# Kernel optimization log

Hardware: AMD Instinct MI355X
Metric: run time of the kernel (lower is better)

## Reference

```python
import jax, jax.numpy as jnp
import numpy as np

B, S, D, DM, H = 2, 2048, 1024, 1024, 16
DH = D // H
EPS = 1e-5


def layernorm(x, g, b):
    m = jnp.mean(x, axis=-1, keepdims=True)
    v = jnp.mean(jnp.square(x - m), axis=-1, keepdims=True)
    return (x - m) * jax.lax.rsqrt(v + EPS) * g + b


def setup_inputs() -> dict:
    key = jax.random.key(0)
    ks = jax.random.split(key, 16)
    std = 0.02
    p = {
        'x': jax.random.normal(ks[0], (B, S, D), jnp.float32),
        'h': jnp.zeros((B, DM), jnp.float32),
        'c': jnp.zeros((B, DM), jnp.float32),
        'Wq': jax.random.normal(ks[1], (D, D), jnp.float32) * std,
        'Wk': jax.random.normal(ks[2], (D, D), jnp.float32) * std,
        'Wv': jax.random.normal(ks[3], (D, D), jnp.float32) * std,
        'Wo': jax.random.normal(ks[4], (D, D), jnp.float32) * std,
        'Wmk': jax.random.normal(ks[5], (DM, D), jnp.float32) * std,
        'Wmv': jax.random.normal(ks[6], (DM, D), jnp.float32) * std,
        'Wih': jax.random.normal(ks[7], (D, 4 * DM), jnp.float32) * std,
        'Whh': jax.random.normal(ks[8], (DM, 4 * DM), jnp.float32) * std,
        'b_ih': jnp.zeros((4 * DM,), jnp.float32),
        'b_hh': jnp.zeros((4 * DM,), jnp.float32),
        'W1': jax.random.normal(ks[9], (D, 4 * D), jnp.float32) * std,
        'bf1': jnp.zeros((4 * D,), jnp.float32),
        'W2': jax.random.normal(ks[10], (4 * D, D), jnp.float32) * std,
        'bf2': jnp.zeros((D,), jnp.float32),
        'g1': jnp.ones((D,), jnp.float32), 'be1': jnp.zeros((D,), jnp.float32),
        'g2': jnp.ones((D,), jnp.float32), 'be2': jnp.zeros((D,), jnp.float32),
        'g3': jnp.ones((D,), jnp.float32), 'be3': jnp.zeros((D,), jnp.float32),
        'Wmp': jax.random.normal(ks[11], (DM, D), jnp.float32) * std,
    }
    return p


def reference(x, h, c, Wq, Wk, Wv, Wo, Wmk, Wmv, Wih, Whh, b_ih, b_hh,
              W1, bf1, W2, bf2, g1, be1, g2, be2, g3, be3, Wmp):
    xn = layernorm(x, g1, be1)
    # projections, split heads: [B,S,D] -> [B,H,S,DH]
    def heads(t):
        return t.reshape(B, -1, H, DH).transpose(0, 2, 1, 3)
    Q = heads(xn @ Wq)
    Ks = heads(xn @ Wk)
    Vs = heads(xn @ Wv)
    Km = (h @ Wmk).reshape(B, 1, H, DH).transpose(0, 2, 1, 3)  # [B,H,1,DH]
    Vm = (h @ Wmv).reshape(B, 1, H, DH).transpose(0, 2, 1, 3)
    K = jnp.concatenate([Km, Ks], axis=2)  # [B,H,S+1,DH]
    V = jnp.concatenate([Vm, Vs], axis=2)
    scores = jnp.einsum('bhqd,bhkd->bhqk', Q, K) / jnp.sqrt(jnp.float32(DH))
    attn = jax.nn.softmax(scores, axis=-1)
    ao = jnp.einsum('bhqk,bhkd->bhqd', attn, V)
    ao = ao.transpose(0, 2, 1, 3).reshape(B, S, D)
    attended = x + ao @ Wo
    # LSTM step on mean-pooled tokens (torch LSTMCell gate order: i,f,g,o)
    pooled = jnp.mean(attended, axis=1)  # [B,D]
    gates = pooled @ Wih + b_ih + h @ Whh + b_hh
    i, f, g, o = jnp.split(gates, 4, axis=-1)
    new_c = jax.nn.sigmoid(f) * c + jax.nn.sigmoid(i) * jnp.tanh(g)
    new_h = jax.nn.sigmoid(o) * jnp.tanh(new_c)
    mixed = attended + (new_h @ Wmp)[:, None, :]
    hn = layernorm(mixed, g2, be2)
    ffn = jax.nn.gelu(hn @ W1 + bf1, approximate=False) @ W2 + bf2
    out = layernorm(mixed + ffn, g3, be3)
    return (out, new_h, new_c)
```

## Files before the change

### kernel.cpp

```cpp
#include <hip/hip_runtime.h>
#include <hip/hip_bf16.h>
#include <math.h>

#define BB 2
#define SS 2048
#define DD 1024
#define HH 16
#define RR (BB*SS)
#define KSTRIDE 2064
#define MB (1024ull*1024ull)

typedef unsigned short u16;
typedef unsigned int u32;
typedef __attribute__((ext_vector_type(8))) short short8v;
typedef __attribute__((ext_vector_type(4))) float f32x4;
typedef __attribute__((ext_vector_type(16))) float f32x16;
typedef __attribute__((ext_vector_type(4))) u16 u16x4;

__device__ __forceinline__ u16 f2bf(float f){
    union { __hip_bfloat16 h; u16 u; } c; c.h = __float2bfloat16(f); return c.u;
}
__device__ __forceinline__ u32 cvtpk(float a, float b){
    u32 r;
    asm("v_cvt_pk_bf16_f32 %0, %1, %2" : "=v"(r) : "v"(a), "v"(b));
    return r;
}
__device__ __forceinline__ float exp2_raw(float x){
    float r;
    asm("v_exp_f32 %0, %1" : "=v"(r) : "v"(x));
    return r;
}
__device__ __forceinline__ float bf2f(u16 u){
    union { u32 i; float f; } c; c.i = (u32)u << 16; return c.f;
}
__device__ __forceinline__ float erf_fast(float x){
    float ax = fabsf(x);
    float t = __builtin_amdgcn_rcpf(1.0f + 0.3275911f*ax);
    float y = t*(0.254829592f + t*(-0.284496736f + t*(1.421413741f + t*(-1.453152027f + t*1.061405429f))));
    float r = 1.0f - y*__expf(-ax*ax);
    return copysignf(r, x);
}

#define GLL16(gp, lp) __builtin_amdgcn_global_load_lds( \
    (const __attribute__((address_space(1))) void*)(gp), \
    (__attribute__((address_space(3))) void*)(lp), 16, 0, 0)

#define VMCNT8 asm volatile("s_waitcnt vmcnt(8)" ::: "memory")
#define VMCNT4 asm volatile("s_waitcnt vmcnt(4)" ::: "memory")
#define VMCNT0 asm volatile("s_waitcnt vmcnt(0)" ::: "memory")
#define SBAR   __builtin_amdgcn_s_barrier()
#define SCHEDB __builtin_amdgcn_sched_barrier(0)

__global__ __launch_bounds__(256) void ln_kernel(const float* __restrict__ in,
    const float* __restrict__ mproj, const float* __restrict__ g, const float* __restrict__ be,
    float* __restrict__ mixed_out, float* __restrict__ outf, u16* __restrict__ outb)
{
    int row = blockIdx.x; int b = row / SS; int tid = threadIdx.x;
    float4 v = ((const float4*)(in + (size_t)row*DD))[tid];
    if (mproj){
        float4 mp = ((const float4*)(mproj + (size_t)b*DD))[tid];
        v.x+=mp.x; v.y+=mp.y; v.z+=mp.z; v.w+=mp.w;
        ((float4*)(mixed_out + (size_t)row*DD))[tid] = v;
    }
    float s = v.x+v.y+v.z+v.w, s2 = v.x*v.x+v.y*v.y+v.z*v.z+v.w*v.w;
    #pragma unroll
    for (int off=32; off>0; off>>=1){ s += __shfl_down(s,off); s2 += __shfl_down(s2,off); }
    __shared__ float red[2][4];
    if ((tid&63)==0){ red[0][tid>>6]=s; red[1][tid>>6]=s2; }
    __syncthreads();
    float st = red[0][0]+red[0][1]+red[0][2]+red[0][3];
    float s2t= red[1][0]+red[1][1]+red[1][2]+red[1][3];
    float mean = st*(1.f/DD); float var = s2t*(1.f/DD)-mean*mean;
    float rs = rsqrtf(var + 1e-5f);
    float4 gg=((const float4*)g)[tid], bb2=((const float4*)be)[tid];
    float o0=(v.x-mean)*rs*gg.x+bb2.x, o1=(v.y-mean)*rs*gg.y+bb2.y;
    float o2=(v.z-mean)*rs*gg.z+bb2.z, o3=(v.w-mean)*rs*gg.w+bb2.w;
    if (outf){ float4 o={o0,o1,o2,o3}; ((float4*)(outf+(size_t)row*DD))[tid]=o; }
    if (outb){ u16x4 o={f2bf(o0),f2bf(o1),f2bf(o2),f2bf(o3)}; ((u16x4*)(outb+(size_t)row*DD))[tid]=o; }
}

__global__ __launch_bounds__(256) void ln3f_kernel(const u16* __restrict__ pb0,
    const u16* __restrict__ pb1, const u16* __restrict__ pb2, const u16* __restrict__ pb3,
    const float* __restrict__ bias, const float* __restrict__ resid,
    const float* __restrict__ g, const float* __restrict__ be, float* __restrict__ out)
{
    int row = blockIdx.x; int tid = threadIdx.x;
    size_t off = (size_t)row*DD;
    u16x4 q0 = ((const u16x4*)(pb0+off))[tid];
    u16x4 q1 = ((const u16x4*)(pb1+off))[tid];
    u16x4 q2 = ((const u16x4*)(pb2+off))[tid];
    u16x4 q3 = ((const u16x4*)(pb3+off))[tid];
    float4 bi = ((const float4*)bias)[tid];
    float4 rs4= ((const float4*)(resid+off))[tid];
    float4 v;
    v.x = bf2f(q0[0])+bf2f(q1[0])+bf2f(q2[0])+bf2f(q3[0]) + bi.x + rs4.x;
    v.y = bf2f(q0[1])+bf2f(q1[1])+bf2f(q2[1])+bf2f(q3[1]) + bi.y + rs4.y;
    v.z = bf2f(q0[2])+bf2f(q1[2])+bf2f(q2[2])+bf2f(q3[2]) + bi.z + rs4.z;
    v.w = bf2f(q0[3])+bf2f(q1[3])+bf2f(q2[3])+bf2f(q3[3]) + bi.w + rs4.w;
    float s = v.x+v.y+v.z+v.w, s2 = v.x*v.x+v.y*v.y+v.z*v.z+v.w*v.w;
    #pragma unroll
    for (int off2=32; off2>0; off2>>=1){ s += __shfl_down(s,off2); s2 += __shfl_down(s2,off2); }
    __shared__ float red[2][4];
    if ((tid&63)==0){ red[0][tid>>6]=s; red[1][tid>>6]=s2; }
    __syncthreads();
    float st = red[0][0]+red[0][1]+red[0][2]+red[0][3];
    float s2t= red[1][0]+red[1][1]+red[1][2]+red[1][3];
    float mean = st*(1.f/DD); float var = s2t*(1.f/DD)-mean*mean;
    float rs = rsqrtf(var + 1e-5f);
    float4 gg=((const float4*)g)[tid], bb2=((const float4*)be)[tid];
    float4 o;
    o.x=(v.x-mean)*rs*gg.x+bb2.x; o.y=(v.y-mean)*rs*gg.y+bb2.y;
    o.z=(v.z-mean)*rs*gg.z+bb2.z; o.w=(v.w-mean)*rs*gg.w+bb2.w;
    ((float4*)(out + off))[tid] = o;
}

__global__ __launch_bounds__(256) void tr6_kernel(const float* __restrict__ Wq, const float* __restrict__ Wk,
    const float* __restrict__ Wv, const float* __restrict__ Wo,
    const float* __restrict__ W1, const float* __restrict__ W2,
    u16* __restrict__ WqkvT, u16* __restrict__ WoT, u16* __restrict__ W1T, u16* __restrict__ W2T)
{
    __shared__ float t[32][33];
    int bid = blockIdx.x;
    const float* in; u16* out; int K, N, n0, k0;
    if (bid < 3072){
        int m = bid >> 10, r = bid & 1023;
        in = (m==0) ? Wq : (m==1) ? Wk : Wv;
        out = WqkvT + (size_t)m*1024*1024;
        K = 1024; N = 1024; n0 = (r & 31)*32; k0 = (r >> 5)*32;
    } else if (bid < 4096){
        int r = bid - 3072;
        in = Wo; out = WoT; K = 1024; N = 1024; n0 = (r & 31)*32; k0 = (r >> 5)*32;
    } else if (bid < 8192){
        int r = bid - 4096;
        in = W1; out = W1T; K = 1024; N = 4096; n0 = (r & 127)*32; k0 = (r >> 7)*32;
    } else {
        int r = bid - 8192;
        in = W2; out = W2T; K = 4096; N = 1024; n0 = (r & 31)*32; k0 = (r >> 5)*32;
    }
    int tx = threadIdx.x & 31, ty = threadIdx.x >> 5;
    #pragma unroll
    for (int i=0;i<4;i++){ int k = ty + i*8; t[k][tx] = in[(size_t)(k0+k)*N + n0 + tx]; }
    __syncthreads();
    #pragma unroll
    for (int i=0;i<4;i++){ int n = ty + i*8; out[(size_t)(n0+n)*K + k0 + tx] = f2bf(t[tx][n]); }
}

__global__ __launch_bounds__(512) void mgemm256(const u16* __restrict__ A, const u16* __restrict__ BT,
    int nbx, int Kc, int kchunks, int mode, const float* __restrict__ bias, float scale,
    void* __restrict__ Cout, void* __restrict__ C2a, void* __restrict__ C2b, void* __restrict__ C2c)
{
    __shared__ __align__(16) u16 lds[2][2][2][256*32];
    int tid = threadIdx.x, l = tid&63, w = tid>>6;
    int wr = w>>2, wc = w&3;
    int nwg = gridDim.x, q8 = nwg>>3;
    int bid = blockIdx.x;
    int swz = (bid & 7)*q8 + (bid >> 3);
    int tiles = nwg / kchunks;
    int chunk = swz / tiles;
    int t2 = swz % tiles;
    int by = t2 / nbx, bx = t2 % nbx;
    int bm = by*256, bn = bx*256;
    int lda = Kc*kchunks;
    int koff = chunk*Kc;
    const int NT = Kc >> 6;

    f32x4 acc[8][4];
    #pragma unroll
    for (int i=0;i<8;i++)
        #pragma unroll
        for (int j=0;j<4;j++)
            #pragma unroll
            for (int r=0;r<4;r++) acc[i][j][r]=0.f;

    auto stage_plane = [&](int buf, int op, int ks, int tt){
        const u16* base = op ? BT : A;
        int tile0 = op ? bn : bm;
        #pragma unroll
        for (int i=0;i<2;i++){
            int rbase = (w*2+i)*16;
            int row = rbase + (l>>2);
            int slotlog = (l&3) ^ ((row>>1)&3);
            const u16* g = base + (size_t)(tile0 + row)*lda + koff + tt*64 + ks*32 + slotlog*8;
            GLL16(g, (u16*)&lds[buf][op][ks][0] + rbase*32);
        }
    };
    auto ds_a = [&](int buf, int ks, int ai) -> short8v {
        int row = wr*128 + ai*16 + (l&15);
        int slot = (l>>4) ^ ((row>>1)&3);
        return *(const short8v*)((const char*)&lds[buf][0][ks][0] + row*64 + slot*16);
    };
    auto ds_b = [&](int buf, int ks, int bi) -> short8v {
        int row = wc*64 + bi*16 + (l&15);
        int slot = (l>>4) ^ ((row>>1)&3);
        return *(const short8v*)((const char*)&lds[buf][1][ks][0] + row*64 + slot*16);
    };

    stage_plane(0,0,0,0); stage_plane(0,1,0,0);
    stage_plane(0,0,1,0); stage_plane(0,1,1,0);
    stage_plane(1,0,0,1); stage_plane(1,1,0,1);
    VMCNT8;
    SBAR; SCHEDB;

    for (int t=0; t<NT; t++){
        int buf = t&1, obuf = buf^1;
        bool s1 = (t+1 < NT), s2 = (t+2 < NT);
        short8v b0,b1,b2,b3, a0,a1,a2,a3;
        b0=ds_b(buf,0,0); b1=ds_b(buf,0,1); b2=ds_b(buf,0,2); b3=ds_b(buf,0,3);
        a0=ds_a(buf,0,0); a1=ds_a(buf,0,1); a2=ds_a(buf,0,2); a3=ds_a(buf,0,3);
        if (s1) stage_plane(obuf,0,1,t+1);
        __builtin_amdgcn_s_setprio(1);
        acc[0][0]=__builtin_amdgcn_mfma_f32_16x16x32_bf16(b0,a0,acc[0][0],0,0,0);
        acc[0][1]=__builtin_amdgcn_mfma_f32_16x16x32_bf16(b1,a0,acc[0][1],0,0,0);
        acc[0][2]=__builtin_amdgcn_mfma_f32_16x16x32_bf16(b2,a0,acc[0][2],0,0,0);
        acc[0][3]=__builtin_amdgcn_mfma_f32_16x16x32_bf16(b3,a0,acc[0][3],0,0,0);
        acc[1][0]=__builtin_amdgcn_mfma_f32_16x16x32_bf16(b0,a1,acc[1][0],0,0,0);
        acc[1][1]=__builtin_amdgcn_mfma_f32_16x16x32_bf16(b1,a1,acc[1][1],0,0,0);
        acc[1][2]=__builtin_amdgcn_mfma_f32_16x16x32_bf16(b2,a1,acc[1][2],0,0,0);
        acc[1][3]=__builtin_amdgcn_mfma_f32_16x16x32_bf16(b3,a1,acc[1][3],0,0,0);
        acc[2][0]=__builtin_amdgcn_mfma_f32_16x16x32_bf16(b0,a2,acc[2][0],0,0,0);
        acc[2][1]=__builtin_amdgcn_mfma_f32_16x16x32_bf16(b1,a2,acc[2][1],0,0,0);
        acc[2][2]=__builtin_amdgcn_mfma_f32_16x16x32_bf16(b2,a2,acc[2][2],0,0,0);
        acc[2][3]=__builtin_amdgcn_mfma_f32_16x16x32_bf16(b3,a2,acc[2][3],0,0,0);
        acc[3][0]=__builtin_amdgcn_mfma_f32_16x16x32_bf16(b0,a3,acc[3][0],0,0,0);
        acc[3][1]=__builtin_amdgcn_mfma_f32_16x16x32_bf16(b1,a3,acc[3][1],0,0,0);
        acc[3][2]=__builtin_amdgcn_mfma_f32_16x16x32_bf16(b2,a3,acc[3][2],0,0,0);
        acc[3][3]=__builtin_amdgcn_mfma_f32_16x16x32_bf16(b3,a3,acc[3][3],0,0,0);
        __builtin_amdgcn_s_setprio(0);
        SBAR; SCHEDB;
        a0=ds_a(buf,0,4); a1=ds_a(buf,0,5); a2=ds_a(buf,0,6); a3=ds_a(buf,0,7);
        if (s1) stage_plane(obuf,1,1,t+1);
        __builtin_amdgcn_s_setprio(1);
        acc[4][0]=__builtin_amdgcn_mfma_f32_16x16x32_bf16(b0,a0,acc[4][0],0,0,0);
        acc[4][1]=__builtin_amdgcn_mfma_f32_16x16x32_bf16(b1,a0,acc[4][1],0,0,0);
        acc[4][2]=__builtin_amdgcn_mfma_f32_16x16x32_bf16(b2,a0,acc[4][2],0,0,0);
        acc[4][3]=__builtin_amdgcn_mfma_f32_16x16x32_bf16(b3,a0,acc[4][3],0,0,0);
        acc[5][0]=__builtin_amdgcn_mfma_f32_16x16x32_bf16(b0,a1,acc[5][0],0,0,0);
        acc[5][1]=__builtin_amdgcn_mfma_f32_16x16x32_bf16(b1,a1,acc[5][1],0,0,0);
        acc[5][2]=__builtin_amdgcn_mfma_f32_16x16x32_bf16(b2,a1,acc[5][2],0,0,0);
        acc[5][3]=__builtin_amdgcn_mfma_f32_16x16x32_bf16(b3,a1,acc[5][3],0,0,0);
        acc[6][0]=__builtin_amdgcn_mfma_f32_16x16x32_bf16(b0,a2,acc[6][0],0,0,0);
        acc[6][1]=__builtin_amdgcn_mfma_f32_16x16x32_bf16(b1,a2,acc[6][1],0,0,0);
        acc[6][2]=__builtin_amdgcn_mfma_f32_16x16x32_bf16(b2,a2,acc[6][2],0,0,0);
        acc[6][3]=__builtin_amdgcn_mfma_f32_16x16x32_bf16(b3,a2,acc[6][3],0,0,0);
        acc[7][0]=__builtin_amdgcn_mfma_f32_16x16x32_bf16(b0,a3,acc[7][0],0,0,0);
        acc[7][1]=__builtin_amdgcn_mfma_f32_16x16x32_bf16(b1,a3,acc[7][1],0,0,0);
        acc[7][2]=__builtin_amdgcn_mfma_f32_16x16x32_bf16(b2,a3,acc[7][2],0,0,0);
        acc[7][3]=__builtin_amdgcn_mfma_f32_16x16x32_bf16(b3,a3,acc[7][3],0,0,0);
        __builtin_amdgcn_s_setprio(0);
        if (s1) { VMCNT8; } else { VMCNT0; }
        SBAR; SCHEDB;
        b0=ds_b(buf,1,0); b1=ds_b(buf,1,1); b2=ds_b(buf,1,2); b3=ds_b(buf,1,3);
        a0=ds_a(buf,1,0); a1=ds_a(buf,1,1); a2=ds_a(buf,1,2); a3=ds_a(buf,1,3);
        if (s2) stage_plane(buf,0,0,t+2);
        __builtin_amdgcn_s_setprio(1);
        acc[0][0]=__builtin_amdgcn_mfma_f32_16x16x32_bf16(b0,a0,acc[0][0],0,0,0);
        acc[0][1]=__builtin_amdgcn_mfma_f32_16x16x32_bf16(b1,a0,acc[0][1],0,0,0);
        acc[0][2]=__builtin_amdgcn_mfma_f32_16x16x32_bf16(b2,a0,acc[0][2],0,0,0);
        acc[0][3]=__builtin_amdgcn_mfma_f32_16x16x32_bf16(b3,a0,acc[0][3],0,0,0);
        acc[1][0]=__builtin_amdgcn_mfma_f32_16x16x32_bf16(b0,a1,acc[1][0],0,0,0);
        acc[1][1]=__builtin_amdgcn_mfma_f32_16x16x32_bf16(b1,a1,acc[1][1],0,0,0);
        acc[1][2]=__builtin_amdgcn_mfma_f32_16x16x32_bf16(b2,a1,acc[1][2],0,0,0);
        acc[1][3]=__builtin_amdgcn_mfma_f32_16x16x32_bf16(b3,a1,acc[1][3],0,0,0);
        acc[2][0]=__builtin_amdgcn_mfma_f32_16x16x32_bf16(b0,a2,acc[2][0],0,0,0);
        acc[2][1]=__builtin_amdgcn_mfma_f32_16x16x32_bf16(b1,a2,acc[2][1],0,0,0);
        acc[2][2]=__builtin_amdgcn_mfma_f32_16x16x32_bf16(b2,a2,acc[2][2],0,0,0);
        acc[2][3]=__builtin_amdgcn_mfma_f32_16x16x32_bf16(b3,a2,acc[2][3],0,0,0);
        acc[3][0]=__builtin_amdgcn_mfma_f32_16x16x32_bf16(b0,a3,acc[3][0],0,0,0);
        acc[3][1]=__builtin_amdgcn_mfma_f32_16x16x32_bf16(b1,a3,acc[3][1],0,0,0);
        acc[3][2]=__builtin_amdgcn_mfma_f32_16x16x32_bf16(b2,a3,acc[3][2],0,0,0);
        acc[3][3]=__builtin_amdgcn_mfma_f32_16x16x32_bf16(b3,a3,acc[3][3],0,0,0);
        __builtin_amdgcn_s_setprio(0);
        SBAR; SCHEDB;
        a0=ds_a(buf,1,4); a1=ds_a(buf,1,5); a2=ds_a(buf,1,6); a3=ds_a(buf,1,7);
        if (s2) stage_plane(buf,1,0,t+2);
        __builtin_amdgcn_s_setprio(1);
        acc[4][0]=__builtin_amdgcn_mfma_f32_16x16x32_bf16(b0,a0,acc[4][0],0,0,0);
        acc[4][1]=__builtin_amdgcn_mfma_f32_16x16x32_bf16(b1,a0,acc[4][1],0,0,0);
        acc[4][2]=__builtin_amdgcn_mfma_f32_16x16x32_bf16(b2,a0,acc[4][2],0,0,0);
        acc[4][3]=__builtin_amdgcn_mfma_f32_16x16x32_bf16(b3,a0,acc[4][3],0,0,0);
        acc[5][0]=__builtin_amdgcn_mfma_f32_16x16x32_bf16(b0,a1,acc[5][0],0,0,0);
        acc[5][1]=__builtin_amdgcn_mfma_f32_16x16x32_bf16(b1,a1,acc[5][1],0,0,0);
        acc[5][2]=__builtin_amdgcn_mfma_f32_16x16x32_bf16(b2,a1,acc[5][2],0,0,0);
        acc[5][3]=__builtin_amdgcn_mfma_f32_16x16x32_bf16(b3,a1,acc[5][3],0,0,0);
        acc[6][0]=__builtin_amdgcn_mfma_f32_16x16x32_bf16(b0,a2,acc[6][0],0,0,0);
        acc[6][1]=__builtin_amdgcn_mfma_f32_16x16x32_bf16(b1,a2,acc[6][1],0,0,0);
        acc[6][2]=__builtin_amdgcn_mfma_f32_16x16x32_bf16(b2,a2,acc[6][2],0,0,0);
        acc[6][3]=__builtin_amdgcn_mfma_f32_16x16x32_bf16(b3,a2,acc[6][3],0,0,0);
        acc[7][0]=__builtin_amdgcn_mfma_f32_16x16x32_bf16(b0,a3,acc[7][0],0,0,0);
        acc[7][1]=__builtin_amdgcn_mfma_f32_16x16x32_bf16(b1,a3,acc[7][1],0,0,0);
        acc[7][2]=__builtin_amdgcn_mfma_f32_16x16x32_bf16(b2,a3,acc[7][2],0,0,0);
        acc[7][3]=__builtin_amdgcn_mfma_f32_16x16x32_bf16(b3,a3,acc[7][3],0,0,0);
        __builtin_amdgcn_s_setprio(0);
        if (s2) { VMCNT8; } else if (s1) { VMCNT4; } else { VMCNT0; }
        SBAR; SCHEDB;
    }

    int N = nbx*256;
    #pragma unroll
    for (int ai=0; ai<8; ai++){
        int m = bm + wr*128 + ai*16 + (l&15);
        #pragma unroll
        for (int bi=0; bi<4; bi++){
            int nb = bn + wc*64 + bi*16 + ((l>>4)<<2);
            f32x4 v = acc[ai][bi];
            if (mode == 0){
                float4 bv = *(const float4*)(bias + nb);
                float t0=v[0]+bv.x, t1=v[1]+bv.y, t2=v[2]+bv.z, t3=v[3]+bv.w;
                u16x4 o;
                o[0]=f2bf(0.5f*t0*(1.0f+erf_fast(t0*0.70710678118654752f)));
                o[1]=f2bf(0.5f*t1*(1.0f+erf_fast(t1*0.70710678118654752f)));
                o[2]=f2bf(0.5f*t2*(1.0f+erf_fast(t2*0.70710678118654752f)));
                o[3]=f2bf(0.5f*t3*(1.0f+erf_fast(t3*0.70710678118654752f)));
                *(u16x4*)((u16*)Cout + (size_t)m*N + nb) = o;
            } else if (mode == 1){
                if (nb < 1024){
                    u16x4 o;
                    #pragma unroll
                    for (int r=0;r<4;r++) o[r] = f2bf(v[r]*scale);
                    *(u16x4*)((u16*)Cout + (size_t)m*1024 + nb) = o;
                } else if (nb < 2048){
                    int cc = nb-1024; int hh = cc>>6, dh = cc&63;
                    int b2 = m>>11, key = m&2047;
                    u16x4 o;
                    #pragma unroll
                    for (int r=0;r<4;r++) o[r] = f2bf(v[r]);
                    *(u16x4*)((u16*)C2a + ((size_t)(b2*HH+hh)*KSTRIDE + key)*64 + dh) = o;
                } else {
                    int cc = nb-2048; int hh = cc>>6, dh = cc&63;
                    int b2 = m>>11, key = m&2047;
                    #pragma unroll
                    for (int r=0;r<4;r++)
                        ((u16*)C2b)[((size_t)(b2*HH+hh)*64 + dh + r)*KSTRIDE + key] = f2bf(v[r]);
                }
            } else {
                u16* pp = (chunk==0) ? (u16*)Cout : (chunk==1) ? (u16*)C2a :
                          (chunk==2) ? (u16*)C2b : (u16*)C2c;
                u16x4 o;
                #pragma unroll
                for (int r=0;r<4;r++) o[r] = f2bf(v[r]);
                *(u16x4*)(pp + (size_t)m*N + nb) = o;
            }
        }
    }
}

#define MODE_F32R 3

__global__ __launch_bounds__(256) void mgemm(const u16* __restrict__ A, const u16* __restrict__ BT,
    int nbx, int Kc, int kchunks, int mode,
    const float* __restrict__ bias, const float* __restrict__ resid, float scale,
    void* __restrict__ Cout, void* __restrict__ C2a, void* __restrict__ C2b)
{
    int tid=threadIdx.x, l=tid&63, w=tid>>6;
    int nwg = gridDim.x;
    int qq = nwg >> 3;
    int bid = blockIdx.x;
    int swz = (bid & 7)*qq + (bid >> 3);
    int tiles = nwg / kchunks;
    int chunk = swz / tiles;
    int t2 = swz % tiles;
    int sby = t2 / (nbx*8);
    int rem = t2 - sby*(nbx*8);
    int sbx = rem >> 6;
    int ci  = rem & 63;
    int bx = sbx*8 + (ci&7);
    int by = sby*8 + (ci>>3);

    int bm = by*128, bn = bx*128;
    int N = nbx*128;
    int lda = Kc*kchunks;
    int koff = chunk*Kc;
    int wr = w>>1, wc = w&1;
    f32x4 acc[4][4];
    #pragma unroll
    for(int i=0;i<4;i++)
        #pragma unroll
        for(int j=0;j<4;j++)
            #pragma unroll
            for(int r=0;r<4;r++) acc[i][j][r]=0.f;

    __shared__ __align__(16) u16 Al[2][4096];
    __shared__ __align__(16) u16 Bl[2][4096];
    int srow = (w<<4) + (l>>2);
    int sph  = l&3;
    const int NT = Kc >> 5;

    auto stage = [&](int buf, int kt){
        #pragma unroll
        for (int r=0;r<2;r++){
            int rowA = srow + r*64;
            int sl = sph ^ ((rowA>>1)&3);
            const u16* gA = A + (size_t)(bm+rowA)*lda + koff + kt*32 + sl*8;
            GLL16(gA, (char*)&Al[buf][0] + r*4096 + w*1024);
            const u16* gB = BT + (size_t)(bn+rowA)*lda + koff + kt*32 + sl*8;
            GLL16(gB, (char*)&Bl[buf][0] + r*4096 + w*1024);
        }
    };

    int cur=0;
    stage(0,0);
    __syncthreads();
    for (int kt=0; kt<NT; kt++){
        if (kt+1<NT) stage(cur^1, kt+1);
        short8v af[4], bf[4];
        #pragma unroll
        for (int mi=0;mi<4;mi++){
            int row = wr*64 + mi*16 + (l&15);
            int sl = (l>>4) ^ ((row>>1)&3);
            af[mi] = *(const short8v*)((const char*)&Al[cur][0] + row*64 + sl*16);
        }
        #pragma unroll
        for (int ni=0;ni<4;ni++){
            int row = wc*64 + ni*16 + (l&15);
            int sl = (l>>4) ^ ((row>>1)&3);
            bf[ni] = *(const short8v*)((const char*)&Bl[cur][0] + row*64 + sl*16);
        }
        #pragma unroll
        for (int mi=0;mi<4;mi++)
            #pragma unroll
            for (int ni=0;ni<4;ni++)
                acc[mi][ni] = __builtin_amdgcn_mfma_f32_16x16x32_bf16(bf[ni], af[mi], acc[mi][ni], 0,0,0);
        __syncthreads();
        cur ^= 1;
    }

    #pragma unroll
    for (int mi=0;mi<4;mi++){
        int m = bm + wr*64 + mi*16 + (l&15);
        #pragma unroll
        for (int ni=0;ni<4;ni++){
            int nb = bn + wc*64 + ni*16 + ((l>>4)<<2);
            f32x4 v = acc[mi][ni];
            float4 rs = *(const float4*)(resid + (size_t)m*N + nb);
            float4 o = {v[0]+rs.x, v[1]+rs.y, v[2]+rs.z, v[3]+rs.w};
            *(float4*)((float*)Cout + (size_t)m*N + nb) = o;
        }
    }
}

__global__ __launch_bounds__(256) void attn_mfma(const u16* __restrict__ Qb, const u16* __restrict__ Kb,
    const u16* __restrict__ VTb, u16* __restrict__ ao)
{
    __shared__ __align__(16) u16 Kl[3][4096];
    __shared__ __align__(16) u16 Vl[3][4096];
    int tid=threadIdx.x, l=tid&63, w=tid>>6;
    int l31=l&31, hi=l>>5;
    int bid = blockIdx.x;
    int xcd = bid & 7, idx = bid >> 3;
    int bh = xcd*4 + (idx>>4);
    int qt = idx & 15;
    int b=bh>>4, h=bh&15;
    int qrow = qt*128 + w*32 + l31;

    const u16* qptr = Qb + (size_t)(b*SS + qrow)*DD + h*64;
    short8v qf[4];
    #pragma unroll
    for (int t=0;t<4;t++) qf[t] = *(const short8v*)(qptr + t*16 + hi*8);

    f32x16 so0, so1;
    #pragma unroll
    for (int i=0;i<16;i++){ so0[i]=0.f; so1[i]=0.f; }
    float l_run=0.f;

    int skey = (w<<3) + (l>>3);
    int ssl  = l&7;
    auto stage = [&](int buf, int kt){
        #pragma unroll
        for (int r=0;r<2;r++){
            int key = skey + r*32;
            int slot = ssl ^ (key&7);
            const u16* gK = Kb + ((size_t)bh*KSTRIDE + kt*64 + key)*64 + slot*8;
            GLL16(gK, (char*)&Kl[buf][0] + r*4096 + w*1024);
            const u16* gV = VTb + ((size_t)bh*64 + key)*KSTRIDE + kt*64 + slot*8;
            GLL16(gV, (char*)&Vl[buf][0] + r*4096 + w*1024);
        }
    };

    auto QK = [&](int bf, f32x16& s0, f32x16& s1){
        #pragma unroll
        for (int i=0;i<16;i++){ s0[i]=0.f; s1[i]=0.f; }
        __builtin_amdgcn_s_setprio(1);
        #pragma unroll
        for (int t=0;t<4;t++){
            int sl = (2*t+hi) ^ (l31&7);
            short8v kf0 = *(const short8v*)((const char*)&Kl[bf][0] + l31*128 + sl*16);
            s0 = __builtin_amdgcn_mfma_f32_32x32x16_bf16(kf0, qf[t], s0, 0,0,0);
            short8v kf1 = *(const short8v*)((const char*)&Kl[bf][0] + (32+l31)*128 + sl*16);
            s1 = __builtin_amdgcn_mfma_f32_32x32x16_bf16(kf1, qf[t], s1, 0,0,0);
        }
        __builtin_amdgcn_s_setprio(0);
    };

    auto SMPV = [&](int bf, f32x16& s0, f32x16& s1){
        float psum = 0.f;
        #pragma unroll
        for (int r=0;r<16;r++){
            float p=exp2_raw(s0[r]); s0[r]=p; psum+=p;
            float q=exp2_raw(s1[r]); s1[r]=q; psum+=q;
        }
        psum += __shfl_xor(psum, 32);
        l_run += psum;
        short8v pf[4];
        #pragma unroll
        for (int t=0;t<4;t++){
            u32 a0,a1,b0,b1;
            if (t==0){ a0=cvtpk(s0[0],s0[1]);   a1=cvtpk(s0[2],s0[3]);   b0=cvtpk(s0[4],s0[5]);   b1=cvtpk(s0[6],s0[7]); }
            else if (t==1){ a0=cvtpk(s0[8],s0[9]);   a1=cvtpk(s0[10],s0[11]); b0=cvtpk(s0[12],s0[13]); b1=cvtpk(s0[14],s0[15]); }
            else if (t==2){ a0=cvtpk(s1[0],s1[1]);   a1=cvtpk(s1[2],s1[3]);   b0=cvtpk(s1[4],s1[5]);   b1=cvtpk(s1[6],s1[7]); }
            else          { a0=cvtpk(s1[8],s1[9]);   a1=cvtpk(s1[10],s1[11]); b0=cvtpk(s1[12],s1[13]); b1=cvtpk(s1[14],s1[15]); }
            union { u32 u[4]; short8v v; } cvt;
#if __has_builtin(__builtin_amdgcn_permlane32_swap)
            auto r0 = __builtin_amdgcn_permlane32_swap(a0, b0, false, false);
            auto r1 = __builtin_amdgcn_permlane32_swap(a1, b1, false, false);
            cvt.u[0] = (u32)r0[0];
            cvt.u[1] = (u32)r1[0];
            cvt.u[2] = (u32)r0[1];
            cvt.u[3] = (u32)r1[1];
#else
            u32 sx0 = hi ? a0 : b0, sx1 = hi ? a1 : b1;
            u32 r0 = (u32)__shfl_xor((int)sx0, 32);
            u32 r1 = (u32)__shfl_xor((int)sx1, 32);
            cvt.u[0] = hi ? r0 : a0;
            cvt.u[1] = hi ? r1 : a1;
            cvt.u[2] = hi ? b0 : r0;
            cvt.u[3] = hi ? b1 : r1;
#endif
            pf[t] = cvt.v;
        }
        __builtin_amdgcn_s_setprio(1);
        #pragma unroll
        for (int t=0;t<4;t++){
            int sl = (2*t+hi) ^ (l31&7);
            short8v vf0 = *(const short8v*)((const char*)&Vl[bf][0] + l31*128 + sl*16);
            so0 = __builtin_amdgcn_mfma_f32_32x32x16_bf16(vf0, pf[t], so0, 0,0,0);
            short8v vf1 = *(const short8v*)((const char*)&Vl[bf][0] + (32+l31)*128 + sl*16);
            so1 = __builtin_amdgcn_mfma_f32_32x32x16_bf16(vf1, pf[t], so1, 0,0,0);
        }
        __builtin_amdgcn_s_setprio(0);
    };

    const int NTILE = 33;
    int bufA = 0, bufB = 1, bufC = 2;
    stage(0, 0);
    stage(1, 1);
    __syncthreads();

    f32x16 sA0, sA1, sB0, sB1;
    QK(bufA, sA0, sA1);

    auto ITER = [&](f32x16& c0, f32x16& c1, f32x16& n0, f32x16& n1, int t){
        if (t+2 < NTILE) stage(bufC, t+2);
        QK(bufB, n0, n1);
        SMPV(bufA, c0, c1);
        __syncthreads();
        int tmp = bufA; bufA = bufB; bufB = bufC; bufC = tmp;
    };
    #pragma unroll 1
    for (int tt=0; tt<16; tt++){
        ITER(sA0, sA1, sB0, sB1, 2*tt);
        ITER(sB0, sB1, sA0, sA1, 2*tt+1);
    }
    #pragma unroll
    for (int r=0;r<16;r++){
        int k0 = 2048 + (r&3) + 8*(r>>2) + 4*hi;
        if (k0 >= 2049) sA0[r] = -1e30f;
        sA1[r] = -1e30f;
    }
    SMPV(bufA, sA0, sA1);

    float inv = 1.f / l_run;
    u16* aop = ao + (size_t)(b*SS + qrow)*DD + h*64;
    #pragma unroll
    for (int rg=0; rg<4; rg++){
        int dh0 = rg*8 + 4*hi;
        u16x4 o0, o1;
        #pragma unroll
        for (int j=0;j<4;j++){ o0[j]=f2bf(so0[rg*4+j]*inv); o1[j]=f2bf(so1[rg*4+j]*inv); }
        *(u16x4*)(aop + dh0) = o0;
        *(u16x4*)(aop + 32 + dh0) = o1;
    }
}

__global__ __launch_bounds__(256) void vecmat_part(const float* __restrict__ vec,
    const float* __restrict__ W, float* __restrict__ part, int K, int N)
{
    int b = blockIdx.z, kc = blockIdx.y;
    int j = blockIdx.x*256 + threadIdx.x;
    int k0 = kc * (K >> 3);
    float acc = 0.0f;
    #pragma unroll 4
    for (int k = k0; k < k0 + (K >> 3); k++)
        acc += vec[(size_t)b*K + k] * W[(size_t)k*N + j];
    part[((size_t)b*8 + kc)*N + j] = acc;
}

__global__ __launch_bounds__(256) void vecmat_red(const float* __restrict__ part,
    float* __restrict__ out, int N)
{
    int b = blockIdx.y;
    int j = blockIdx.x*256 + threadIdx.x;
    float acc = 0.0f;
    #pragma unroll
    for (int kc = 0; kc < 8; kc++) acc += part[((size_t)b*8 + kc)*N + j];
    out[(size_t)b*N + j] = acc;
}

__global__ __launch_bounds__(256) void vecmat2_part(const float* __restrict__ vec,
    const float* __restrict__ Wa, const float* __restrict__ Wb, float* __restrict__ part)
{
    int b = blockIdx.z, kc = blockIdx.y;
    int j = blockIdx.x*256 + threadIdx.x;
    int k0 = kc * 128;
    float accA = 0.0f, accB = 0.0f;
    #pragma unroll 4
    for (int k = k0; k < k0 + 128; k++){
        float v = vec[(size_t)b*DD + k];
        accA += v * Wa[(size_t)k*DD + j];
        accB += v * Wb[(size_t)k*DD + j];
    }
    part[((size_t)b*8 + kc)*2048 + j] = accA;
    part[((size_t)b*8 + kc)*2048 + 1024 + j] = accB;
}

__global__ __launch_bounds__(256) void fixup_kernel(const float* __restrict__ v2part,
    u16* __restrict__ Kb, u16* __restrict__ VTb)
{
    int idx = blockIdx.x*256 + threadIdx.x;
    int b = idx>>10, j = idx&1023; int h=j>>6, dh=j&63; int bh=b*HH+h;
    float km = 0.f, vm = 0.f;
    #pragma unroll
    for (int kc = 0; kc < 8; kc++){
        km += v2part[((size_t)b*8 + kc)*2048 + j];
        vm += v2part[((size_t)b*8 + kc)*2048 + 1024 + j];
    }
    Kb[((size_t)bh*KSTRIDE + 2048)*64 + dh] = f2bf(km);
    VTb[((size_t)bh*64 + dh)*KSTRIDE + 2048] = f2bf(vm);
}

__global__ __launch_bounds__(256) void pool1_kernel(const float* __restrict__ att, float* __restrict__ ppart)
{
    int b = blockIdx.y, sc = blockIdx.x;
    int tid = threadIdx.x;
    float4 acc = {0,0,0,0};
    for (int s = 0; s < 32; s++) {
        int row = b*SS + sc*32 + s;
        float4 v = ((const float4*)(att + (size_t)row*DD))[tid];
        acc.x += v.x; acc.y += v.y; acc.z += v.z; acc.w += v.w;
    }
    ((float4*)(ppart + ((size_t)b*64 + sc)*DD))[tid] = acc;
}

__global__ __launch_bounds__(256) void pool2_kernel(const float* __restrict__ ppart, float* __restrict__ pooled)
{
    int b = blockIdx.y;
    int j = blockIdx.x*256 + threadIdx.x;
    float acc = 0.0f;
    for (int sc = 0; sc < 64; sc++) acc += ppart[((size_t)b*64 + sc)*DD + j];
    pooled[(size_t)b*DD + j] = acc * (1.0f/SS);
}

__global__ __launch_bounds__(256) void gates_part(const float* __restrict__ pooled,
    const float* __restrict__ h, const float* __restrict__ Wih, const float* __restrict__ Whh,
    float* __restrict__ part)
{
    int b = blockIdx.z, kc = blockIdx.y;
    int j = blockIdx.x*256 + threadIdx.x;
    int k0 = kc * 64;
    float acc = 0.0f;
    #pragma unroll 4
    for (int k = k0; k < k0 + 64; k++)
        acc += pooled[(size_t)b*DD + k] * Wih[(size_t)k*4*DD + j]
             + h[(size_t)b*DD + k]      * Whh[(size_t)k*4*DD + j];
    part[((size_t)b*16 + kc)*4*DD + j] = acc;
}

__device__ __forceinline__ float sigmoidf_(float x) { return 1.0f / (1.0f + __expf(-x)); }

__global__ __launch_bounds__(256) void lstm_kernel(const float* __restrict__ gpart,
    const float* __restrict__ b_ih, const float* __restrict__ b_hh,
    const float* __restrict__ c, float* __restrict__ newh_ws, float* __restrict__ out_tail)
{
    int idx = blockIdx.x*256 + threadIdx.x;
    int b = idx >> 10, d = idx & 1023;
    float sI = b_ih[d]          + b_hh[d];
    float sF = b_ih[DD + d]     + b_hh[DD + d];
    float sG = b_ih[2*DD + d]   + b_hh[2*DD + d];
    float sO = b_ih[3*DD + d]   + b_hh[3*DD + d];
    #pragma unroll
    for (int kc = 0; kc < 16; kc++){
        const float* gp = gpart + ((size_t)b*16 + kc)*4*DD;
        sI += gp[d]; sF += gp[DD + d]; sG += gp[2*DD + d]; sO += gp[3*DD + d];
    }
    float ig = sigmoidf_(sI);
    float fg = sigmoidf_(sF);
    float gg = tanhf(sG);
    float og = sigmoidf_(sO);
    float nc = fg * c[idx] + ig * gg;
    float nh = og * tanhf(nc);
    newh_ws[idx] = nh;
    out_tail[idx] = nh;
    out_tail[BB*DD + idx] = nc;
}

extern "C" void kernel_launch(void* const* d_in, const int* in_sizes, int n_in,
                              void* d_out, int out_size, void* d_ws, size_t ws_size,
                              hipStream_t stream) {
    const float* x    = (const float*)d_in[0];
    const float* h    = (const float*)d_in[1];
    const float* c    = (const float*)d_in[2];
    const float* Wq   = (const float*)d_in[3];
    const float* Wk   = (const float*)d_in[4];
    const float* Wv   = (const float*)d_in[5];
    const float* Wo   = (const float*)d_in[6];
    const float* Wmk  = (const float*)d_in[7];
    const float* Wmv  = (const float*)d_in[8];
    const float* Wih  = (const float*)d_in[9];
    const float* Whh  = (const float*)d_in[10];
    const float* b_ih = (const float*)d_in[11];
    const float* b_hh = (const float*)d_in[12];
    const float* W1   = (const float*)d_in[13];
    const float* bf1  = (const float*)d_in[14];
    const float* W2   = (const float*)d_in[15];
    const float* bf2  = (const float*)d_in[16];
    const float* g1   = (const float*)d_in[17];
    const float* be1  = (const float*)d_in[18];
    const float* g2   = (const float*)d_in[19];
    const float* be2  = (const float*)d_in[20];
    const float* g3   = (const float*)d_in[21];
    const float* be3  = (const float*)d_in[22];
    const float* Wmp  = (const float*)d_in[23];

    float* out = (float*)d_out;
    char* wsb  = (char*)d_ws;

    u16*   xn   = (u16*)(wsb + 0);
    u16*   hn   = (u16*)(wsb + 8*MB);
    u16*   pb0  = (u16*)(wsb + 0);
    u16*   pb1  = (u16*)(wsb + 8*MB);
    u16*   Qbuf = (u16*)(wsb + 16*MB);
    u16*   Kbuf = (u16*)(wsb + 24*MB);
    u16*   VTb  = (u16*)(wsb + 33*MB);
    u16*   act  = (u16*)(wsb + 16*MB);
    u16*   ao   = (u16*)(wsb + 48*MB);
    u16*   pb2  = (u16*)(wsb + 48*MB);
    float* attb = (float*)(wsb + 56*MB);
    u16*   WqkvT= (u16*)(wsb + 72*MB);
    u16*   WoT  = (u16*)(wsb + 78*MB);
    u16*   W1T  = (u16*)(wsb + 80*MB);
    u16*   pb3  = (u16*)(wsb + 80*MB);
    u16*   W2T  = (u16*)(wsb + 88*MB);
    float* sm   = (float*)(wsb + 96*MB);
    float* pooled  = sm;
    float* newh    = pooled + 2048;
    float* mproj   = newh + 2048;
    float* vpart   = mproj + 2048;
    float* v2part  = vpart + 16384;
    float* gpart   = v2part + 32768;
    float* ppart   = gpart + 131072;

    tr6_kernel<<<12288, 256, 0, stream>>>(Wq, Wk, Wv, Wo, W1, W2, WqkvT, WoT, W1T, W2T);

    ln_kernel<<<RR, 256, 0, stream>>>(x, nullptr, g1, be1, nullptr, nullptr, xn);
    vecmat2_part<<<dim3(4,8,BB), 256, 0, stream>>>(h, Wmk, Wmv, v2part);
    mgemm256<<<192, 512, 0, stream>>>(xn, WqkvT, 12, 1024, 1, 1, nullptr,
                                      0.125f*1.44269504088896f, Qbuf, Kbuf, VTb, nullptr);
    fixup_kernel<<<8, 256, 0, stream>>>(v2part, Kbuf, VTb);
    attn_mfma<<<512, 256, 0, stream>>>(Qbuf, Kbuf, VTb, ao);
    mgemm<<<8*32, 256, 0, stream>>>(ao, WoT, 8, 1024, 1, MODE_F32R, nullptr, x, 1.f, attb, nullptr, nullptr);
    pool1_kernel<<<dim3(64,BB), 256, 0, stream>>>(attb, ppart);
    pool2_kernel<<<dim3(4,BB), 256, 0, stream>>>(ppart, pooled);
    gates_part<<<dim3(16,16,BB), 256, 0, stream>>>(pooled, h, Wih, Whh, gpart);
    lstm_kernel<<<8, 256, 0, stream>>>(gpart, b_ih, b_hh, c, newh, out + (size_t)RR*DD);
    vecmat_part<<<dim3(4,8,BB), 256, 0, stream>>>(newh, Wmp, vpart, DD, DD);
    vecmat_red<<<dim3(4,BB), 256, 0, stream>>>(vpart, mproj, DD);
    ln_kernel<<<RR, 256, 0, stream>>>(attb, mproj, g2, be2, attb, nullptr, hn);
    mgemm256<<<256, 512, 0, stream>>>(hn, W1T, 16, 1024, 1, 0, bf1, 1.f, act, nullptr, nullptr, nullptr);
    mgemm256<<<256, 512, 0, stream>>>(act, W2T, 4, 1024, 4, 2, nullptr, 1.f, pb0, pb1, pb2, pb3);
    ln3f_kernel<<<RR, 256, 0, stream>>>(pb0, pb1, pb2, pb3, bf2, attb, g3, be3, out);
}
```

Before: 279.8 us.

## Split attention over key halves and split-K the output projection

The attention kernel now splits the key range into two halves, doubling the grid to 1024 blocks. Each half writes unnormalized fp32 partial outputs and its row sums, and a new combine kernel normalizes and merges them into the bf16 attention output. The Wo projection drops the dedicated 128-tile GEMM and uses the 256-thread-tile GEMM with a 4-way K split into bf16 partials. A new reduction kernel then sums those partials and adds the residual x. The aim is better CU occupancy and parallelism, at the cost of extra fp32/bf16 intermediate traffic, two more launches, and some precision loss from bf16 partial sums.

```diff
diff --git a/kernel.cpp b/kernel.cpp
--- a/kernel.cpp
+++ b/kernel.cpp
@@ -112,6 +112,44 @@
     o.x=(v.x-mean)*rs*gg.x+bb2.x; o.y=(v.y-mean)*rs*gg.y+bb2.y;
     o.z=(v.z-mean)*rs*gg.z+bb2.z; o.w=(v.w-mean)*rs*gg.w+bb2.w;
     ((float4*)(out + off))[tid] = o;
+}
+
+__global__ __launch_bounds__(256) void wored_kernel(const u16* __restrict__ p0,
+    const u16* __restrict__ p1, const u16* __restrict__ p2, const u16* __restrict__ p3,
+    const float* __restrict__ x, float* __restrict__ attb)
+{
+    int row = blockIdx.x; int tid = threadIdx.x;
+    size_t off = (size_t)row*DD;
+    u16x4 q0 = ((const u16x4*)(p0+off))[tid];
+    u16x4 q1 = ((const u16x4*)(p1+off))[tid];
+    u16x4 q2 = ((const u16x4*)(p2+off))[tid];
+    u16x4 q3 = ((const u16x4*)(p3+off))[tid];
+    float4 xv = ((const float4*)(x+off))[tid];
+    float4 o;
+    o.x = bf2f(q0[0])+bf2f(q1[0])+bf2f(q2[0])+bf2f(q3[0]) + xv.x;
+    o.y = bf2f(q0[1])+bf2f(q1[1])+bf2f(q2[1])+bf2f(q3[1]) + xv.y;
+    o.z = bf2f(q0[2])+bf2f(q1[2])+bf2f(q2[2])+bf2f(q3[2]) + xv.z;
+    o.w = bf2f(q0[3])+bf2f(q1[3])+bf2f(q2[3])+bf2f(q3[3]) + xv.w;
+    ((float4*)(attb+off))[tid] = o;
+}
+
+__global__ __launch_bounds__(256) void attcomb_kernel(const float* __restrict__ O0,
+    const float* __restrict__ O1, const float* __restrict__ lp,
+    u16* __restrict__ ao)
+{
+    int row = blockIdx.x; int tid = threadIdx.x;
+    int b = row >> 11, qr = row & 2047;
+    int h = tid >> 4;
+    size_t off = (size_t)row*DD + tid*4;
+    float l0 = lp[(size_t)(b*HH+h)*SS + qr];
+    float l1 = lp[(size_t)65536 + (size_t)(b*HH+h)*SS + qr];
+    float inv = 1.0f / (l0 + l1);
+    float4 a = *(const float4*)(O0 + off);
+    float4 c = *(const float4*)(O1 + off);
+    u16x4 o;
+    o[0]=f2bf((a.x+c.x)*inv); o[1]=f2bf((a.y+c.y)*inv);
+    o[2]=f2bf((a.z+c.z)*inv); o[3]=f2bf((a.w+c.w)*inv);
+    *(u16x4*)(ao + off) = o;
 }
 
 __global__ __launch_bounds__(256) void tr6_kernel(const float* __restrict__ Wq, const float* __restrict__ Wk,
@@ -344,102 +382,8 @@
     }
 }
 
-#define MODE_F32R 3
-
-__global__ __launch_bounds__(256) void mgemm(const u16* __restrict__ A, const u16* __restrict__ BT,
-    int nbx, int Kc, int kchunks, int mode,
-    const float* __restrict__ bias, const float* __restrict__ resid, float scale,
-    void* __restrict__ Cout, void* __restrict__ C2a, void* __restrict__ C2b)
-{
-    int tid=threadIdx.x, l=tid&63, w=tid>>6;
-    int nwg = gridDim.x;
-    int qq = nwg >> 3;
-    int bid = blockIdx.x;
-    int swz = (bid & 7)*qq + (bid >> 3);
-    int tiles = nwg / kchunks;
-    int chunk = swz / tiles;
-    int t2 = swz % tiles;
-    int sby = t2 / (nbx*8);
-    int rem = t2 - sby*(nbx*8);
-    int sbx = rem >> 6;
-    int ci  = rem & 63;
-    int bx = sbx*8 + (ci&7);
-    int by = sby*8 + (ci>>3);
-
-    int bm = by*128, bn = bx*128;
-    int N = nbx*128;
-    int lda = Kc*kchunks;
-    int koff = chunk*Kc;
-    int wr = w>>1, wc = w&1;
-    f32x4 acc[4][4];
-    #pragma unroll
-    for(int i=0;i<4;i++)
-        #pragma unroll
-        for(int j=0;j<4;j++)
-            #pragma unroll
-            for(int r=0;r<4;r++) acc[i][j][r]=0.f;
-
-    __shared__ __align__(16) u16 Al[2][4096];
-    __shared__ __align__(16) u16 Bl[2][4096];
-    int srow = (w<<4) + (l>>2);
-    int sph  = l&3;
-    const int NT = Kc >> 5;
-
-    auto stage = [&](int buf, int kt){
-        #pragma unroll
-        for (int r=0;r<2;r++){
-            int rowA = srow + r*64;
-            int sl = sph ^ ((rowA>>1)&3);
-            const u16* gA = A + (size_t)(bm+rowA)*lda + koff + kt*32 + sl*8;
-            GLL16(gA, (char*)&Al[buf][0] + r*4096 + w*1024);
-            const u16* gB = BT + (size_t)(bn+rowA)*lda + koff + kt*32 + sl*8;
-            GLL16(gB, (char*)&Bl[buf][0] + r*4096 + w*1024);
-        }
-    };
-
-    int cur=0;
-    stage(0,0);
-    __syncthreads();
-    for (int kt=0; kt<NT; kt++){
-        if (kt+1<NT) stage(cur^1, kt+1);
-        short8v af[4], bf[4];
-        #pragma unroll
-        for (int mi=0;mi<4;mi++){
-            int row = wr*64 + mi*16 + (l&15);
-            int sl = (l>>4) ^ ((row>>1)&3);
-            af[mi] = *(const short8v*)((const char*)&Al[cur][0] + row*64 + sl*16);
-        }
-        #pragma unroll
-        for (int ni=0;ni<4;ni++){
-            int row = wc*64 + ni*16 + (l&15);
-            int sl = (l>>4) ^ ((row>>1)&3);
-            bf[ni] = *(const short8v*)((const char*)&Bl[cur][0] + row*64 + sl*16);
-        }
-        #pragma unroll
-        for (int mi=0;mi<4;mi++)
-            #pragma unroll
-            for (int ni=0;ni<4;ni++)
-                acc[mi][ni] = __builtin_amdgcn_mfma_f32_16x16x32_bf16(bf[ni], af[mi], acc[mi][ni], 0,0,0);
-        __syncthreads();
-        cur ^= 1;
-    }
-
-    #pragma unroll
-    for (int mi=0;mi<4;mi++){
-        int m = bm + wr*64 + mi*16 + (l&15);
-        #pragma unroll
-        for (int ni=0;ni<4;ni++){
-            int nb = bn + wc*64 + ni*16 + ((l>>4)<<2);
-            f32x4 v = acc[mi][ni];
-            float4 rs = *(const float4*)(resid + (size_t)m*N + nb);
-            float4 o = {v[0]+rs.x, v[1]+rs.y, v[2]+rs.z, v[3]+rs.w};
-            *(float4*)((float*)Cout + (size_t)m*N + nb) = o;
-        }
-    }
-}
-
 __global__ __launch_bounds__(256) void attn_mfma(const u16* __restrict__ Qb, const u16* __restrict__ Kb,
-    const u16* __restrict__ VTb, u16* __restrict__ ao)
+    const u16* __restrict__ VTb, float* __restrict__ O0, float* __restrict__ O1, float* __restrict__ lp)
 {
     __shared__ __align__(16) u16 Kl[3][4096];
     __shared__ __align__(16) u16 Vl[3][4096];
@@ -447,10 +391,13 @@
     int l31=l&31, hi=l>>5;
     int bid = blockIdx.x;
     int xcd = bid & 7, idx = bid >> 3;
-    int bh = xcd*4 + (idx>>4);
+    int half = idx >> 6;
+    int bh = xcd*4 + ((idx>>4)&3);
     int qt = idx & 15;
     int b=bh>>4, h=bh&15;
     int qrow = qt*128 + w*32 + l31;
+    int kt0 = half*16;
+    const int NTILE = half ? 17 : 16;
 
     const u16* qptr = Qb + (size_t)(b*SS + qrow)*DD + h*64;
     short8v qf[4];
@@ -469,9 +416,9 @@
         for (int r=0;r<2;r++){
             int key = skey + r*32;
             int slot = ssl ^ (key&7);
-            const u16* gK = Kb + ((size_t)bh*KSTRIDE + kt*64 + key)*64 + slot*8;
+            const u16* gK = Kb + ((size_t)bh*KSTRIDE + (kt0+kt)*64 + key)*64 + slot*8;
             GLL16(gK, (char*)&Kl[buf][0] + r*4096 + w*1024);
-            const u16* gV = VTb + ((size_t)bh*64 + key)*KSTRIDE + kt*64 + slot*8;
+            const u16* gV = VTb + ((size_t)bh*64 + key)*KSTRIDE + (kt0+kt)*64 + slot*8;
             GLL16(gV, (char*)&Vl[buf][0] + r*4096 + w*1024);
         }
     };
@@ -539,7 +486,6 @@
         __builtin_amdgcn_s_setprio(0);
     };
 
-    const int NTILE = 33;
     int bufA = 0, bufB = 1, bufC = 2;
     stage(0, 0);
     stage(1, 1);
@@ -555,29 +501,42 @@
         __syncthreads();
         int tmp = bufA; bufA = bufB; bufB = bufC; bufC = tmp;
     };
-    #pragma unroll 1
-    for (int tt=0; tt<16; tt++){
-        ITER(sA0, sA1, sB0, sB1, 2*tt);
-        ITER(sB0, sB1, sA0, sA1, 2*tt+1);
-    }
-    #pragma unroll
-    for (int r=0;r<16;r++){
-        int k0 = 2048 + (r&3) + 8*(r>>2) + 4*hi;
-        if (k0 >= 2049) sA0[r] = -1e30f;
-        sA1[r] = -1e30f;
-    }
-    SMPV(bufA, sA0, sA1);
-
-    float inv = 1.f / l_run;
-    u16* aop = ao + (size_t)(b*SS + qrow)*DD + h*64;
+
+    if (half == 0){
+        #pragma unroll 1
+        for (int tt=0; tt<7; tt++){
+            ITER(sA0, sA1, sB0, sB1, 2*tt);
+            ITER(sB0, sB1, sA0, sA1, 2*tt+1);
+        }
+        ITER(sA0, sA1, sB0, sB1, 14);
+        SMPV(bufA, sB0, sB1);
+    } else {
+        #pragma unroll 1
+        for (int tt=0; tt<8; tt++){
+            ITER(sA0, sA1, sB0, sB1, 2*tt);
+            ITER(sB0, sB1, sA0, sA1, 2*tt+1);
+        }
+        #pragma unroll
+        for (int r=0;r<16;r++){
+            int k0 = 2048 + (r&3) + 8*(r>>2) + 4*hi;
+            if (k0 >= 2049) sA0[r] = -1e30f;
+            sA1[r] = -1e30f;
+        }
+        SMPV(bufA, sA0, sA1);
+    }
+
+    float* Op = half ? O1 : O0;
+    float* op = Op + (size_t)(b*SS + qrow)*DD + h*64;
     #pragma unroll
     for (int rg=0; rg<4; rg++){
         int dh0 = rg*8 + 4*hi;
-        u16x4 o0, o1;
-        #pragma unroll
-        for (int j=0;j<4;j++){ o0[j]=f2bf(so0[rg*4+j]*inv); o1[j]=f2bf(so1[rg*4+j]*inv); }
-        *(u16x4*)(aop + dh0) = o0;
-        *(u16x4*)(aop + 32 + dh0) = o1;
+        float4 o0 = {so0[rg*4+0], so0[rg*4+1], so0[rg*4+2], so0[rg*4+3]};
+        float4 o1 = {so1[rg*4+0], so1[rg*4+1], so1[rg*4+2], so1[rg*4+3]};
+        *(float4*)(op + dh0) = o0;
+        *(float4*)(op + 32 + dh0) = o1;
+    }
+    if (!hi){
+        lp[(size_t)half*65536 + (size_t)(b*HH+h)*SS + qt*128 + w*32 + l31] = l_run;
     }
 }
 
@@ -735,15 +694,21 @@
 
     u16*   xn   = (u16*)(wsb + 0);
     u16*   hn   = (u16*)(wsb + 8*MB);
+    float* O0p  = (float*)(wsb + 0);
     u16*   pb0  = (u16*)(wsb + 0);
     u16*   pb1  = (u16*)(wsb + 8*MB);
     u16*   Qbuf = (u16*)(wsb + 16*MB);
     u16*   Kbuf = (u16*)(wsb + 24*MB);
     u16*   VTb  = (u16*)(wsb + 33*MB);
+    u16*   pw0  = (u16*)(wsb + 16*MB);
+    u16*   pw1  = (u16*)(wsb + 24*MB);
+    u16*   pw2  = (u16*)(wsb + 32*MB);
+    u16*   pw3  = (u16*)(wsb + 40*MB);
     u16*   act  = (u16*)(wsb + 16*MB);
     u16*   ao   = (u16*)(wsb + 48*MB);
     u16*   pb2  = (u16*)(wsb + 48*MB);
     float* attb = (float*)(wsb + 56*MB);
+    float* O1p  = (float*)(wsb + 56*MB);
     u16*   WqkvT= (u16*)(wsb + 72*MB);
     u16*   WoT  = (u16*)(wsb + 78*MB);
     u16*   W1T  = (u16*)(wsb + 80*MB);
@@ -757,6 +722,7 @@
     float* v2part  = vpart + 16384;
     float* gpart   = v2part + 32768;
     float* ppart   = gpart + 131072;
+    float* lpart   = ppart + 131072;
 
     tr6_kernel<<<12288, 256, 0, stream>>>(Wq, Wk, Wv, Wo, W1, W2, WqkvT, WoT, W1T, W2T);
 
@@ -765,8 +731,10 @@
     mgemm256<<<192, 512, 0, stream>>>(xn, WqkvT, 12, 1024, 1, 1, nullptr,
                                       0.125f*1.44269504088896f, Qbuf, Kbuf, VTb, nullptr);
     fixup_kernel<<<8, 256, 0, stream>>>(v2part, Kbuf, VTb);
-    attn_mfma<<<512, 256, 0, stream>>>(Qbuf, Kbuf, VTb, ao);
-    mgemm<<<8*32, 256, 0, stream>>>(ao, WoT, 8, 1024, 1, MODE_F32R, nullptr, x, 1.f, attb, nullptr, nullptr);
+    attn_mfma<<<1024, 256, 0, stream>>>(Qbuf, Kbuf, VTb, O0p, O1p, lpart);
+    attcomb_kernel<<<RR, 256, 0, stream>>>(O0p, O1p, lpart, ao);
+    mgemm256<<<256, 512, 0, stream>>>(ao, WoT, 4, 256, 4, 2, nullptr, 1.f, pw0, pw1, pw2, pw3);
+    wored_kernel<<<RR, 256, 0, stream>>>(pw0, pw1, pw2, pw3, x, attb);
     pool1_kernel<<<dim3(64,BB), 256, 0, stream>>>(attb, ppart);
     pool2_kernel<<<dim3(4,BB), 256, 0, stream>>>(ppart, pooled);
     gates_part<<<dim3(16,16,BB), 256, 0, stream>>>(pooled, h, Wih, Whh, gpart);
```

After: 298.0 us. 1.06x slower.
